# Performance work log

Measured on AMD Instinct MI355X. Metric: run time of the kernel, lower is better.

The kernel has to match this reference:

```python
import jax, jax.numpy as jnp
import numpy as np

EMB = 1024

def setup_inputs() -> dict:
    key = jax.random.key(0)
    ks = jax.random.split(key, 6)
    T, k1, k2, D = 64, 256, 1024, EMB
    scale = 1.0 / np.sqrt(D)
    return {
        "fast_feature": jax.random.normal(ks[0], (T, k2, D), jnp.float32),
        "slow_feature": jax.random.normal(ks[1], (T, k1, D), jnp.float32),
        "fast_W": jax.random.normal(ks[2], (D, D), jnp.float32) * scale,
        "fast_b": jax.random.normal(ks[3], (D,), jnp.float32) * 0.01,
        "slow_W": jax.random.normal(ks[4], (D, D), jnp.float32) * scale,
        "slow_b": jax.random.normal(ks[5], (D,), jnp.float32) * 0.01,
    }

def reference(fast_feature, slow_feature, fast_W, fast_b, slow_W, slow_b):
    # Linear projections (torch Linear: x @ W.T + b)
    fast_key = jnp.einsum('tkd,ed->tke', fast_feature, fast_W) + fast_b  # [T,k2,D]
    slow_key = jnp.einsum('tkd,ed->tke', slow_feature, slow_W) + slow_b  # [T,k1,D]
    # Scaled dot-product similarity fast->slow
    sim = jnp.einsum('tqd,tkd->tqk', fast_key, slow_key)  # [T,k2,k1]
    sim = sim / jnp.sqrt(jnp.asarray(slow_feature.shape[-1], sim.dtype))
    attn = jax.nn.softmax(sim, axis=-1)
    ctx = jnp.einsum('tqk,tkd->tqd', attn, slow_feature)  # note: values are raw slow_feature
    return fast_feature + ctx
```

## Files before the change

### kernel.cpp

```cpp
#include <hip/hip_runtime.h>
#include <stdint.h>

typedef __attribute__((ext_vector_type(8))) short bf16x8;
typedef __attribute__((ext_vector_type(4))) float f32x4;

__device__ __forceinline__ unsigned short f2bf(float f) {
  unsigned int u = __builtin_bit_cast(unsigned int, f);
  u += 0x7FFFu + ((u >> 16) & 1u);
  return (unsigned short)(u >> 16);
}

__device__ __forceinline__ void gload_lds16(const void* g, void* l) {
  __builtin_amdgcn_global_load_lds(
      (__attribute__((address_space(1))) void*)(uintptr_t)g,
      (__attribute__((address_space(3))) void*)l,
      16, 0, 0);
}

#define BARRIER() do { asm volatile("" ::: "memory"); __builtin_amdgcn_s_barrier(); asm volatile("" ::: "memory"); } while (0)
#define WAITVM(N) asm volatile("s_waitcnt vmcnt(" #N ")" ::: "memory")

template <int MODE>
__global__ __launch_bounds__(512, 2) void gemm8(
    const unsigned short* __restrict__ A, const unsigned short* __restrict__ B,
    void* __restrict__ Cv, const float* __restrict__ aux, int N, int K,
    int nm, int nn, int ntiles, long sAB, long sBB, long sCB, long sXB,
    float scale)
{
  __shared__ __align__(16) char lds[131072];
  char* ldsc = lds;

  const int tid = threadIdx.x;
  const int lane = tid & 63;
  const int wid = tid >> 6;
  const int fr = lane & 15, fq = lane >> 4;

  const int nwg = gridDim.x;
  const int id = blockIdx.x;
  const int swz = (id & 7) * (nwg >> 3) + (id >> 3);
  const int per = nm * nn;
  const int t = swz / per;
  const int rem = swz - t * per;
  const int mi_ = rem / nn, ni_ = rem - mi_ * nn;
  const long bmBase = (long)mi_ * 256 * ntiles;
  const long bn = (long)ni_ * 256;

  const unsigned short* Ag = A + (long)t * sAB + bmBase * K;
  const unsigned short* Bg = B + (long)t * sBB + bn * K;
  const int NT = K >> 6;
  const int lnt = __builtin_ctz(NT);
  const int kmask = NT - 1;
  const int G = ntiles << lnt;
  const long tsA = (long)256 * K;

  const unsigned short* aS[2][2];
  const unsigned short* bS[2][2];
#pragma unroll
  for (int p = 0; p < 2; ++p) {
    const int q = p * 512 + tid;
    const int lr = q >> 3, cs = q & 7;
    const int cl = cs ^ (lr & 7);
#pragma unroll
    for (int h = 0; h < 2; ++h) {
      const int gA = ((lr >> 6) << 7) | (h << 6) | (lr & 63);
      const int gB = ((lr >> 5) << 6) | (h << 5) | (lr & 31);
      aS[p][h] = Ag + (long)gA * K + cl * 8;
      bS[p][h] = Bg + (long)gB * K + cl * 8;
    }
  }

#define AOFF(g) (((long)((g) & kmask) << 6) + (long)((g) >> lnt) * tsA)
#define BOFF(g) ((long)((g) & kmask) << 6)

  const int c0 = ((fq ^ (fr & 3)) + ((fr >> 2) & 1) * 4) * 16;
  const int aRd = ((wid >> 2) * 64 + fr) * 128 + c0;
  const int bRd = ((wid & 3) * 32 + fr) * 128 + c0;

  f32x4 acc[2][2][4][2];
#pragma unroll
  for (int a = 0; a < 2; a++)
#pragma unroll
    for (int b = 0; b < 2; b++)
#pragma unroll
      for (int i = 0; i < 4; i++)
#pragma unroll
        for (int j = 0; j < 2; j++)
#pragma unroll
          for (int r = 0; r < 4; r++) acc[a][b][i][j][r] = 0.f;

  bf16x8 af[4][2], bf[2][2][2];

#define STAGE(srcArr, aoff, h, eoff, b) do {                                  \
  _Pragma("unroll")                                                           \
  for (int p = 0; p < 2; ++p)                                                 \
    gload_lds16(srcArr[p][h] + (eoff),                                        \
                ldsc + (aoff) + ((b) << 16) + ((h) << 14) + (p << 13) + (wid << 10)); \
} while (0)

#define LDA(mi, cub) do {                                                     \
  _Pragma("unroll")                                                           \
  for (int i = 0; i < 4; ++i) {                                               \
    af[i][0] = *(const bf16x8*)(ldsc + (cub) + (mi) * 16384 + aRd + i * 2048);        \
    af[i][1] = *(const bf16x8*)(ldsc + (cub) + (mi) * 16384 + (aRd ^ 64) + i * 2048); \
  }                                                                           \
} while (0)

#define LDB(nj, cub) do {                                                     \
  _Pragma("unroll")                                                           \
  for (int j = 0; j < 2; ++j) {                                               \
    bf[nj][j][0] = *(const bf16x8*)(ldsc + 32768 + (cub) + (nj) * 16384 + bRd + j * 2048);        \
    bf[nj][j][1] = *(const bf16x8*)(ldsc + 32768 + (cub) + (nj) * 16384 + (bRd ^ 64) + j * 2048); \
  }                                                                           \
} while (0)

#define QUAD(mi, nj) do {                                                     \
  __builtin_amdgcn_s_setprio(1);                                              \
  _Pragma("unroll")                                                           \
  for (int i = 0; i < 4; ++i)                                                 \
  _Pragma("unroll")                                                           \
  for (int j = 0; j < 2; ++j) {                                               \
    acc[mi][nj][i][j] = __builtin_amdgcn_mfma_f32_16x16x32_bf16(              \
        af[i][0], bf[nj][j][0], acc[mi][nj][i][j], 0, 0, 0);                  \
    acc[mi][nj][i][j] = __builtin_amdgcn_mfma_f32_16x16x32_bf16(              \
        af[i][1], bf[nj][j][1], acc[mi][nj][i][j], 0, 0, 0);                  \
  }                                                                           \
  __builtin_amdgcn_s_setprio(0);                                              \
} while (0)

  STAGE(aS, 0, 0, AOFF(0), 0);
  STAGE(bS, 32768, 0, BOFF(0), 0);
  STAGE(bS, 32768, 1, BOFF(0), 0);
  STAGE(aS, 0, 1, AOFF(0), 0);
  if (G > 1) {
    STAGE(aS, 0, 0, AOFF(1), 1);
    STAGE(bS, 32768, 0, BOFF(1), 1);
    STAGE(bS, 32768, 1, BOFF(1), 1);
    WAITVM(6);
  } else {
    WAITVM(0);
  }
  BARRIER();

  for (int g = 0; g < G; ++g) {
    const int cur = g & 1, nxt = cur ^ 1;
    const int cub = cur << 16;
    LDA(0, cub);
    LDB(0, cub);
    if (g + 1 < G) STAGE(aS, 0, 1, AOFF(g + 1), nxt);
    BARRIER();
    QUAD(0, 0);
    BARRIER();
    LDB(1, cub);
    if (g + 2 < G) STAGE(aS, 0, 0, AOFF(g + 2), cur);
    BARRIER();
    QUAD(0, 1);
    BARRIER();
    LDA(1, cub);
    if (g + 2 < G) STAGE(bS, 32768, 0, BOFF(g + 2), cur);
    BARRIER();
    QUAD(1, 0);
    BARRIER();
    if (g + 2 < G) {
      STAGE(bS, 32768, 1, BOFF(g + 2), cur);
      QUAD(1, 1);
      WAITVM(6);
    } else {
      QUAD(1, 1);
      WAITVM(0);
    }
    BARRIER();

    if ((g & kmask) != kmask) continue;

    const int s = g >> lnt;
    const long bm = bmBase + (long)s * 256;
    if (MODE == 1) {
      float* red  = (float*)ldsc;
      float* red2 = (float*)(ldsc + 4096);
      const int wc = wid & 3;
      const int rbase = (wid >> 2) * 128;
#pragma unroll
      for (int mi = 0; mi < 2; ++mi)
#pragma unroll
        for (int i = 0; i < 4; ++i)
#pragma unroll
          for (int r = 0; r < 4; ++r) {
            float m = fmaxf(fmaxf(acc[mi][0][i][0][r], acc[mi][0][i][1][r]),
                            fmaxf(acc[mi][1][i][0][r], acc[mi][1][i][1][r]));
#pragma unroll
            for (int o = 1; o <= 8; o <<= 1) m = fmaxf(m, __shfl_xor(m, o));
            if (fr == 0) red[(rbase + mi * 64 + i * 16 + fq * 4 + r) * 4 + wc] = m;
          }
      BARRIER();
#pragma unroll
      for (int mi = 0; mi < 2; ++mi)
#pragma unroll
        for (int i = 0; i < 4; ++i)
#pragma unroll
          for (int r = 0; r < 4; ++r) {
            const int rl = rbase + mi * 64 + i * 16 + fq * 4 + r;
            f32x4 mm = *(f32x4*)&red[rl * 4];
            const float M = fmaxf(fmaxf(mm[0], mm[1]), fmaxf(mm[2], mm[3]));
            float sm = 0.f;
#pragma unroll
            for (int nj = 0; nj < 2; ++nj)
#pragma unroll
              for (int j = 0; j < 2; ++j) {
                float e = __expf((acc[mi][nj][i][j][r] - M) * scale);
                acc[mi][nj][i][j][r] = e;
                sm += e;
              }
#pragma unroll
            for (int o = 1; o <= 8; o <<= 1) sm += __shfl_xor(sm, o);
            if (fr == 0) red2[rl * 4 + wc] = sm;
          }
      BARRIER();
      unsigned short* C = (unsigned short*)Cv + (long)t * sCB;
#pragma unroll
      for (int mi = 0; mi < 2; ++mi)
#pragma unroll
        for (int i = 0; i < 4; ++i)
#pragma unroll
          for (int r = 0; r < 4; ++r) {
            const int rl = rbase + mi * 64 + i * 16 + fq * 4 + r;
            f32x4 sv = *(f32x4*)&red2[rl * 4];
            const float inv = 1.0f / (sv[0] + sv[1] + sv[2] + sv[3]);
            const long gr = bm + rl;
#pragma unroll
            for (int nj = 0; nj < 2; ++nj)
#pragma unroll
              for (int j = 0; j < 2; ++j) {
                const long gcol = bn + wc * 64 + nj * 32 + j * 16 + fr;
                C[gr * N + gcol] = f2bf(acc[mi][nj][i][j][r] * inv);
              }
          }
    } else {
#pragma unroll
      for (int mi = 0; mi < 2; ++mi)
#pragma unroll
        for (int nj = 0; nj < 2; ++nj)
#pragma unroll
          for (int i = 0; i < 4; ++i) {
            const long grow0 = bm + (wid >> 2) * 128 + mi * 64 + i * 16 + fq * 4;
#pragma unroll
            for (int j = 0; j < 2; ++j) {
              const long gcol = bn + (wid & 3) * 64 + nj * 32 + j * 16 + fr;
              if (MODE == 0) {
                unsigned short* C = (unsigned short*)Cv + (long)t * sCB;
                const float bv = aux[gcol];
#pragma unroll
                for (int r = 0; r < 4; ++r)
                  C[(grow0 + r) * N + gcol] = f2bf(acc[mi][nj][i][j][r] + bv);
              } else {
                float* C = (float*)Cv + (long)t * sCB;
                const float* X = aux + (long)t * sXB;
#pragma unroll
                for (int r = 0; r < 4; ++r) {
                  const long idx = (grow0 + r) * N + gcol;
                  C[idx] = acc[mi][nj][i][j][r] + X[idx];
                }
              }
            }
          }
#pragma unroll
      for (int a = 0; a < 2; a++)
#pragma unroll
        for (int b = 0; b < 2; b++)
#pragma unroll
          for (int i = 0; i < 4; i++)
#pragma unroll
            for (int j = 0; j < 2; j++)
#pragma unroll
              for (int r = 0; r < 4; r++) acc[a][b][i][j][r] = 0.f;
    }
  }
#undef STAGE
#undef LDA
#undef LDB
#undef QUAD
#undef AOFF
#undef BOFF
}

__global__ __launch_bounds__(256) void convert_f32_bf16(
    const float* __restrict__ in, unsigned short* __restrict__ out, long n) {
  long i = ((long)blockIdx.x * 256 + threadIdx.x) * 4;
  long stride = (long)gridDim.x * 1024;
  for (; i < n; i += stride) {
    float4 v = *(const float4*)(in + i);
    ushort4 o;
    o.x = f2bf(v.x); o.y = f2bf(v.y); o.z = f2bf(v.z); o.w = f2bf(v.w);
    *(ushort4*)(out + i) = o;
  }
}

__global__ __launch_bounds__(256) void convert_transpose_slow(
    const float* __restrict__ in, unsigned short* __restrict__ outR,
    unsigned short* __restrict__ outT) {
  __shared__ unsigned short tile[32][33];
  int t = blockIdx.z;
  int d0 = blockIdx.x * 32;
  int k0 = blockIdx.y * 32;
  const float* ip = in + (long)t * 256 * 1024;
  unsigned short* rp = outR + (long)t * 256 * 1024;
  unsigned short* tp = outT + (long)t * 1024 * 256;
  int tx = threadIdx.x & 31, ty = threadIdx.x >> 5;
#pragma unroll
  for (int p = 0; p < 4; p++) {
    int k = ty + p * 8;
    unsigned short b = f2bf(ip[(long)(k0 + k) * 1024 + d0 + tx]);
    tile[k][tx] = b;
    rp[(long)(k0 + k) * 1024 + d0 + tx] = b;
  }
  __syncthreads();
#pragma unroll
  for (int p = 0; p < 4; p++) {
    int d = ty + p * 8;
    tp[(long)(d0 + d) * 256 + k0 + tx] = tile[tx][d];
  }
}

extern "C" void kernel_launch(void* const* d_in, const int* in_sizes, int n_in,
                              void* d_out, int out_size, void* d_ws, size_t ws_size,
                              hipStream_t stream) {
  const float* fastF     = (const float*)d_in[0];
  const float* slowF     = (const float*)d_in[1];
  const float* fastW     = (const float*)d_in[2];
  const float* fast_bias = (const float*)d_in[3];
  const float* slowW     = (const float*)d_in[4];
  const float* slow_bias = (const float*)d_in[5];
  float* out = (float*)d_out;

  char* ws = (char*)d_ws;
  unsigned short* fastBf  = (unsigned short*)(ws);
  unsigned short* attnBf  = (unsigned short*)(ws + 67108864L);
  unsigned short* fastKey = (unsigned short*)(ws + 134217728L);
  unsigned short* slowBf  = (unsigned short*)(ws + 268435456L);
  unsigned short* slowT   = (unsigned short*)(ws + 301989888L);
  unsigned short* slowKey = (unsigned short*)(ws + 335544320L);
  unsigned short* fWb     = (unsigned short*)(ws + 369098752L);
  unsigned short* sWb     = (unsigned short*)(ws + 371195904L);

  convert_f32_bf16<<<2048, 256, 0, stream>>>(fastF, fastBf, 67108864L);
  convert_f32_bf16<<<1024, 256, 0, stream>>>(fastW, fWb, 1048576L);
  convert_f32_bf16<<<1024, 256, 0, stream>>>(slowW, sWb, 1048576L);
  convert_transpose_slow<<<dim3(32, 8, 64), 256, 0, stream>>>(slowF, slowBf, slowT);

  gemm8<0><<<256, 512, 0, stream>>>(slowBf, sWb, slowKey, slow_bias,
      1024, 1024, 64, 4, 1, 0, 0, 0, 0, 1.f);
  gemm8<0><<<256, 512, 0, stream>>>(fastBf, fWb, fastKey, fast_bias,
      1024, 1024, 64, 4, 4, 0, 0, 0, 0, 1.f);
  gemm8<1><<<256, 512, 0, stream>>>(fastKey, slowKey, attnBf, nullptr,
      256, 1024, 4, 1, 1, 1048576L, 262144L, 262144L, 0, 0.03125f);
  gemm8<2><<<256, 512, 0, stream>>>(attnBf, slowT, out, fastF,
      1024, 256, 1, 4, 4, 262144L, 262144L, 1048576L, 1048576L, 1.f);
}
```

Before: 552.4 us.

## Load all fragments before MFMAs, split persistent tiles, use bf16 residual

The GEMM main loop now reads all A and B fragments from LDS up front into two A register sets, then runs the MFMA quads with far fewer barriers. The global-to-LDS staging for later k-steps is moved into fewer points. The fast-projection and output GEMMs launch 1024 workgroups with one tile each instead of 256 persistent workgroups with four tiles, to improve load balance. The final residual add reads the bf16 copy of fast_feature instead of the fp32 original, halving that read traffic at the cost of rounding the residual term. The cost is more live registers and reduced precision in the output.

```diff
diff --git a/kernel.cpp b/kernel.cpp
--- a/kernel.cpp
+++ b/kernel.cpp
@@ -8,6 +8,10 @@
   unsigned int u = __builtin_bit_cast(unsigned int, f);
   u += 0x7FFFu + ((u >> 16) & 1u);
   return (unsigned short)(u >> 16);
+}
+
+__device__ __forceinline__ float bf2f(unsigned short s) {
+  return __builtin_bit_cast(float, (unsigned int)s << 16);
 }
 
 __device__ __forceinline__ void gload_lds16(const void* g, void* l) {
@@ -23,7 +27,7 @@
 template <int MODE>
 __global__ __launch_bounds__(512, 2) void gemm8(
     const unsigned short* __restrict__ A, const unsigned short* __restrict__ B,
-    void* __restrict__ Cv, const float* __restrict__ aux, int N, int K,
+    void* __restrict__ Cv, const void* __restrict__ aux, int N, int K,
     int nm, int nn, int ntiles, long sAB, long sBB, long sCB, long sXB,
     float scale)
 {
@@ -88,7 +92,7 @@
 #pragma unroll
           for (int r = 0; r < 4; r++) acc[a][b][i][j][r] = 0.f;
 
-  bf16x8 af[4][2], bf[2][2][2];
+  bf16x8 af0[4][2], af1[4][2], bfr[2][2][2];
 
 #define STAGE(srcArr, aoff, h, eoff, b) do {                                  \
   _Pragma("unroll")                                                           \
@@ -97,32 +101,32 @@
                 ldsc + (aoff) + ((b) << 16) + ((h) << 14) + (p << 13) + (wid << 10)); \
 } while (0)
 
-#define LDA(mi, cub) do {                                                     \
+#define LDA(dst, mi, cub) do {                                                \
   _Pragma("unroll")                                                           \
   for (int i = 0; i < 4; ++i) {                                               \
-    af[i][0] = *(const bf16x8*)(ldsc + (cub) + (mi) * 16384 + aRd + i * 2048);        \
-    af[i][1] = *(const bf16x8*)(ldsc + (cub) + (mi) * 16384 + (aRd ^ 64) + i * 2048); \
+    dst[i][0] = *(const bf16x8*)(ldsc + (cub) + (mi) * 16384 + aRd + i * 2048);        \
+    dst[i][1] = *(const bf16x8*)(ldsc + (cub) + (mi) * 16384 + (aRd ^ 64) + i * 2048); \
   }                                                                           \
 } while (0)
 
 #define LDB(nj, cub) do {                                                     \
   _Pragma("unroll")                                                           \
   for (int j = 0; j < 2; ++j) {                                               \
-    bf[nj][j][0] = *(const bf16x8*)(ldsc + 32768 + (cub) + (nj) * 16384 + bRd + j * 2048);        \
-    bf[nj][j][1] = *(const bf16x8*)(ldsc + 32768 + (cub) + (nj) * 16384 + (bRd ^ 64) + j * 2048); \
+    bfr[nj][j][0] = *(const bf16x8*)(ldsc + 32768 + (cub) + (nj) * 16384 + bRd + j * 2048);        \
+    bfr[nj][j][1] = *(const bf16x8*)(ldsc + 32768 + (cub) + (nj) * 16384 + (bRd ^ 64) + j * 2048); \
   }                                                                           \
 } while (0)
 
-#define QUAD(mi, nj) do {                                                     \
+#define QUAD(AF, mi, nj) do {                                                 \
   __builtin_amdgcn_s_setprio(1);                                              \
   _Pragma("unroll")                                                           \
   for (int i = 0; i < 4; ++i)                                                 \
   _Pragma("unroll")                                                           \
   for (int j = 0; j < 2; ++j) {                                               \
     acc[mi][nj][i][j] = __builtin_amdgcn_mfma_f32_16x16x32_bf16(              \
-        af[i][0], bf[nj][j][0], acc[mi][nj][i][j], 0, 0, 0);                  \
+        AF[i][0], bfr[nj][j][0], acc[mi][nj][i][j], 0, 0, 0);                 \
     acc[mi][nj][i][j] = __builtin_amdgcn_mfma_f32_16x16x32_bf16(              \
-        af[i][1], bf[nj][j][1], acc[mi][nj][i][j], 0, 0, 0);                  \
+        AF[i][1], bfr[nj][j][1], acc[mi][nj][i][j], 0, 0, 0);                 \
   }                                                                           \
   __builtin_amdgcn_s_setprio(0);                                              \
 } while (0)
@@ -142,32 +146,24 @@
   BARRIER();
 
   for (int g = 0; g < G; ++g) {
-    const int cur = g & 1, nxt = cur ^ 1;
+    const int cur = g & 1;
     const int cub = cur << 16;
-    LDA(0, cub);
+    LDA(af0, 0, cub);
     LDB(0, cub);
-    if (g + 1 < G) STAGE(aS, 0, 1, AOFF(g + 1), nxt);
-    BARRIER();
-    QUAD(0, 0);
-    BARRIER();
     LDB(1, cub);
-    if (g + 2 < G) STAGE(aS, 0, 0, AOFF(g + 2), cur);
-    BARRIER();
-    QUAD(0, 1);
-    BARRIER();
-    LDA(1, cub);
-    if (g + 2 < G) STAGE(bS, 32768, 0, BOFF(g + 2), cur);
-    BARRIER();
-    QUAD(1, 0);
+    LDA(af1, 1, cub);
+    if (g + 1 < G) STAGE(aS, 0, 1, AOFF(g + 1), cur ^ 1);
+    QUAD(af0, 0, 0);
+    QUAD(af0, 0, 1);
+    QUAD(af1, 1, 0);
     BARRIER();
     if (g + 2 < G) {
+      STAGE(aS, 0, 0, AOFF(g + 2), cur);
+      STAGE(bS, 32768, 0, BOFF(g + 2), cur);
       STAGE(bS, 32768, 1, BOFF(g + 2), cur);
-      QUAD(1, 1);
-      WAITVM(6);
-    } else {
-      QUAD(1, 1);
-      WAITVM(0);
     }
+    QUAD(af1, 1, 1);
+    if (g + 2 < G) { WAITVM(6); } else { WAITVM(0); }
     BARRIER();
 
     if ((g & kmask) != kmask) continue;
@@ -247,31 +243,33 @@
               const long gcol = bn + (wid & 3) * 64 + nj * 32 + j * 16 + fr;
               if (MODE == 0) {
                 unsigned short* C = (unsigned short*)Cv + (long)t * sCB;
-                const float bv = aux[gcol];
+                const float bv = ((const float*)aux)[gcol];
 #pragma unroll
                 for (int r = 0; r < 4; ++r)
                   C[(grow0 + r) * N + gcol] = f2bf(acc[mi][nj][i][j][r] + bv);
               } else {
                 float* C = (float*)Cv + (long)t * sCB;
-                const float* X = aux + (long)t * sXB;
+                const unsigned short* X = (const unsigned short*)aux + (long)t * sXB;
 #pragma unroll
                 for (int r = 0; r < 4; ++r) {
                   const long idx = (grow0 + r) * N + gcol;
-                  C[idx] = acc[mi][nj][i][j][r] + X[idx];
+                  C[idx] = acc[mi][nj][i][j][r] + bf2f(X[idx]);
                 }
               }
             }
           }
-#pragma unroll
-      for (int a = 0; a < 2; a++)
-#pragma unroll
-        for (int b = 0; b < 2; b++)
-#pragma unroll
-          for (int i = 0; i < 4; i++)
-#pragma unroll
-            for (int j = 0; j < 2; j++)
-#pragma unroll
-              for (int r = 0; r < 4; r++) acc[a][b][i][j][r] = 0.f;
+      if (g + 1 < G) {
+#pragma unroll
+        for (int a = 0; a < 2; a++)
+#pragma unroll
+          for (int b = 0; b < 2; b++)
+#pragma unroll
+            for (int i = 0; i < 4; i++)
+#pragma unroll
+              for (int j = 0; j < 2; j++)
+#pragma unroll
+                for (int r = 0; r < 4; r++) acc[a][b][i][j][r] = 0.f;
+      }
     }
   }
 #undef STAGE
@@ -333,9 +331,9 @@
 
   char* ws = (char*)d_ws;
   unsigned short* fastBf  = (unsigned short*)(ws);
-  unsigned short* attnBf  = (unsigned short*)(ws + 67108864L);
   unsigned short* fastKey = (unsigned short*)(ws + 134217728L);
   unsigned short* slowBf  = (unsigned short*)(ws + 268435456L);
+  unsigned short* attnBf  = (unsigned short*)(ws + 268435456L);
   unsigned short* slowT   = (unsigned short*)(ws + 301989888L);
   unsigned short* slowKey = (unsigned short*)(ws + 335544320L);
   unsigned short* fWb     = (unsigned short*)(ws + 369098752L);
@@ -348,10 +346,10 @@
 
   gemm8<0><<<256, 512, 0, stream>>>(slowBf, sWb, slowKey, slow_bias,
       1024, 1024, 64, 4, 1, 0, 0, 0, 0, 1.f);
-  gemm8<0><<<256, 512, 0, stream>>>(fastBf, fWb, fastKey, fast_bias,
-      1024, 1024, 64, 4, 4, 0, 0, 0, 0, 1.f);
+  gemm8<0><<<1024, 512, 0, stream>>>(fastBf, fWb, fastKey, fast_bias,
+      1024, 1024, 256, 4, 1, 0, 0, 0, 0, 1.f);
   gemm8<1><<<256, 512, 0, stream>>>(fastKey, slowKey, attnBf, nullptr,
       256, 1024, 4, 1, 1, 1048576L, 262144L, 262144L, 0, 0.03125f);
-  gemm8<2><<<256, 512, 0, stream>>>(attnBf, slowT, out, fastF,
-      1024, 256, 1, 4, 4, 262144L, 262144L, 1048576L, 1048576L, 1.f);
-}
+  gemm8<2><<<1024, 512, 0, stream>>>(attnBf, slowT, out, fastBf,
+      1024, 256, 4, 4, 1, 262144L, 262144L, 1048576L, 1048576L, 1.f);
+}
```

New measurement: 685.7 us. +24.1%, slower.
